# Performance work log

Measured on AMD Instinct MI355X. Metric: run time of the kernel, lower is better.

Reference implementation:

```python
import jax, jax.numpy as jnp
import numpy as np

B, S, H, NH = 2, 2048, 2048, 16
HD = H // NH  # head_dim = 128


def setup_inputs() -> dict:
    key = jax.random.key(0)
    ks = jax.random.split(key, 6)
    scale = 1.0 / np.sqrt(H)
    hidden_state = jax.random.normal(ks[0], (B, S, H), dtype=jnp.float32)
    # upper-triangular (strictly above diagonal) = 1 -> masked positions
    causal_mask = jnp.triu(jnp.ones((S, S), dtype=jnp.float32), k=1)[None, None]
    Wq = jax.random.normal(ks[1], (H, H), dtype=jnp.float32) * scale
    Wk = jax.random.normal(ks[2], (H, H), dtype=jnp.float32) * scale
    Wv = jax.random.normal(ks[3], (H, H), dtype=jnp.float32) * scale
    Wo = jax.random.normal(ks[4], (H, H), dtype=jnp.float32) * scale
    zeros = jnp.zeros((H,), dtype=jnp.float32)
    return {"hidden_state": hidden_state, "causal_mask": causal_mask,
            "Wq": Wq, "bq": zeros, "Wk": Wk, "bk": zeros,
            "Wv": Wv, "bv": zeros, "Wo": Wo, "bo": zeros}


def reference(hidden_state, causal_mask, Wq, bq, Wk, bk, Wv, bv, Wo, bo):
    b, s, h = hidden_state.shape
    q = (hidden_state @ Wq.T + bq).reshape(b, s, NH, HD).transpose(0, 2, 1, 3)  # [B,NH,S,HD]
    k = (hidden_state @ Wk.T + bk).reshape(b, s, NH, HD).transpose(0, 2, 1, 3)
    v = (hidden_state @ Wv.T + bv).reshape(b, s, NH, HD).transpose(0, 2, 1, 3)
    scores = jnp.einsum('bhqd,bhkd->bhqk', q, k) / jnp.sqrt(jnp.float32(HD))
    scores = scores + causal_mask * (-1e9)
    probs = jax.nn.softmax(scores, axis=-1)
    out = jnp.einsum('bhqk,bhkd->bhqd', probs, v)
    out = out.transpose(0, 2, 1, 3).reshape(b, s, h)
    return out @ Wo.T + bo
```

## Files before the change

kernel.cpp:

```cpp
#include <hip/hip_runtime.h>
#include <hip/hip_bf16.h>
#include <stdint.h>

#define B_   2
#define S_   2048
#define H_   2048
#define NH_  16
#define HD_  128
#define MTOT (B_*S_)

typedef __attribute__((ext_vector_type(8))) short bf16x8;
typedef __attribute__((ext_vector_type(4))) float f32x4;

__device__ __forceinline__ void gload_lds16(const void* g, void* l) {
    __builtin_amdgcn_global_load_lds(
        (const __attribute__((address_space(1))) void*)g,
        (__attribute__((address_space(3))) void*)l, 16, 0, 0);
}

__device__ __forceinline__ unsigned short f2bfu(float x) {
    __hip_bfloat16 h = __float2bfloat16(x);
    return *reinterpret_cast<unsigned short*>(&h);
}

__global__ void castk(const float* __restrict__ in, __hip_bfloat16* __restrict__ out, int n4) {
    int i = blockIdx.x * 256 + threadIdx.x;
    if (i < n4) {
        float4 v = *(const float4*)(in + (size_t)i * 4);
        out[(size_t)i*4 + 0] = __float2bfloat16(v.x);
        out[(size_t)i*4 + 1] = __float2bfloat16(v.y);
        out[(size_t)i*4 + 2] = __float2bfloat16(v.z);
        out[(size_t)i*4 + 3] = __float2bfloat16(v.w);
    }
}

__global__ void castw4(const float* __restrict__ w0, const float* __restrict__ w1,
                       const float* __restrict__ w2, const float* __restrict__ w3,
                       __hip_bfloat16* o0, __hip_bfloat16* o1,
                       __hip_bfloat16* o2, __hip_bfloat16* o3, int n4) {
    const float* in; __hip_bfloat16* out;
    switch (blockIdx.y) {
        case 0:  in = w0; out = o0; break;
        case 1:  in = w1; out = o1; break;
        case 2:  in = w2; out = o2; break;
        default: in = w3; out = o3; break;
    }
    int i = blockIdx.x * 256 + threadIdx.x;
    if (i < n4) {
        float4 v = *(const float4*)(in + (size_t)i * 4);
        out[(size_t)i*4 + 0] = __float2bfloat16(v.x);
        out[(size_t)i*4 + 1] = __float2bfloat16(v.y);
        out[(size_t)i*4 + 2] = __float2bfloat16(v.z);
        out[(size_t)i*4 + 3] = __float2bfloat16(v.w);
    }
}

template<int OUT_BF16>
__device__ __forceinline__ void gemm_body(const __hip_bfloat16* __restrict__ Ablk,
                                          const __hip_bfloat16* __restrict__ Wblk,
                                          const float* __restrict__ bias,
                                          void* __restrict__ Cout,
                                          int N, int K, int br, int bc)
{
    __shared__ __align__(16) __hip_bfloat16 As[128 * 32];
    __shared__ __align__(16) __hip_bfloat16 Bs[128 * 32];

    const int tid  = threadIdx.x;
    const int wave = tid >> 6, lane = tid & 63;
    const int quad = lane >> 4, l16 = lane & 15;
    const int wr = wave >> 1, wc = wave & 1;

    f32x4 acc[4][4] = {};

    for (int k0 = 0; k0 < K; k0 += 32) {
#pragma unroll
        for (int t = 0; t < 2; ++t) {
            int c = t * 256 + wave * 64 + lane;
            int row = c >> 2, cc = c & 3;
            int base = (t * 256 + wave * 64) * 16;
            gload_lds16(Ablk + (size_t)row * K + k0 + cc * 8, (char*)As + base);
            gload_lds16(Wblk + (size_t)row * K + k0 + cc * 8, (char*)Bs + base);
        }
        __syncthreads();

        bf16x8 af[4], bf[4];
#pragma unroll
        for (int i = 0; i < 4; ++i)
            af[i] = *(const bf16x8*)&As[(wr * 64 + i * 16 + l16) * 32 + quad * 8];
#pragma unroll
        for (int j = 0; j < 4; ++j)
            bf[j] = *(const bf16x8*)&Bs[(wc * 64 + j * 16 + l16) * 32 + quad * 8];

#pragma unroll
        for (int i = 0; i < 4; ++i)
#pragma unroll
            for (int j = 0; j < 4; ++j)
                acc[i][j] = __builtin_amdgcn_mfma_f32_16x16x32_bf16(af[i], bf[j], acc[i][j], 0, 0, 0);
        __syncthreads();
    }

#pragma unroll
    for (int i = 0; i < 4; ++i) {
        int row = br * 128 + wr * 64 + i * 16 + quad * 4;
#pragma unroll
        for (int j = 0; j < 4; ++j) {
            int col = bc * 128 + wc * 64 + j * 16 + l16;
            float bv = bias[col];
#pragma unroll
            for (int r = 0; r < 4; ++r) {
                float v = acc[i][j][r] + bv;
                if (OUT_BF16)
                    ((__hip_bfloat16*)Cout)[(size_t)(row + r) * N + col] = __float2bfloat16(v);
                else
                    ((float*)Cout)[(size_t)(row + r) * N + col] = v;
            }
        }
    }
}

__global__ __launch_bounds__(256)
void gemm_qkv(const __hip_bfloat16* __restrict__ X,
              const __hip_bfloat16* __restrict__ Wq, const __hip_bfloat16* __restrict__ Wk,
              const __hip_bfloat16* __restrict__ Wv,
              const float* __restrict__ bq, const float* __restrict__ bk,
              const float* __restrict__ bv,
              __hip_bfloat16* Qo, __hip_bfloat16* Ko, __hip_bfloat16* Vo)
{
    const int sel = blockIdx.x >> 4;
    const int bc  = blockIdx.x & 15;
    const int br  = blockIdx.y;
    const __hip_bfloat16* W = (sel == 0) ? Wq : (sel == 1) ? Wk : Wv;
    const float* bias       = (sel == 0) ? bq : (sel == 1) ? bk : bv;
    __hip_bfloat16* out     = (sel == 0) ? Qo : (sel == 1) ? Ko : Vo;
    gemm_body<1>(X + (size_t)(br * 128) * H_, W + (size_t)(bc * 128) * H_,
                 bias, out, H_, H_, br, bc);
}

__global__ __launch_bounds__(256)
void gemm_out(const __hip_bfloat16* __restrict__ A, const __hip_bfloat16* __restrict__ W,
              const float* __restrict__ bias, float* __restrict__ C)
{
    gemm_body<0>(A + (size_t)(blockIdx.y * 128) * H_, W + (size_t)(blockIdx.x * 128) * H_,
                 bias, C, H_, H_, blockIdx.y, blockIdx.x);
}

#define VSTR 72
#define PSTR 72

__global__ __launch_bounds__(256)
void attn_kernel(const __hip_bfloat16* __restrict__ Q,
                 const __hip_bfloat16* __restrict__ K,
                 const __hip_bfloat16* __restrict__ V,
                 __hip_bfloat16* __restrict__ O)
{
    __shared__ __align__(16) char KsB[2][64 * 256];
    __shared__ __align__(16) __hip_bfloat16 VsT[128 * VSTR];
    __shared__ __align__(16) __hip_bfloat16 Ps[4][16 * PSTR];

    const int tid  = threadIdx.x;
    const int wave = tid >> 6, lane = tid & 63;
    const int quad = lane >> 4, l16 = lane & 15;

    const int lid  = blockIdx.x;
    const int xcd  = lid & 7;
    const int slot = lid >> 3;
    const int bh   = ((slot >> 4) << 3) | xcd;
    const int pr   = slot & 15;
    const int b    = bh >> 4, h = bh & 15;

    const size_t headoff = (size_t)b * S_ * H_ + (size_t)h * HD_;
    const __hip_bfloat16* Qp = Q + headoff;
    const __hip_bfloat16* Kp = K + headoff;
    const __hip_bfloat16* Vp = V + headoff;

    const float scale = 0.08838834764831843f;

    for (int which = 0; which < 2; ++which) {
        const int qb = which ? pr : 31 - pr;
        const int qrow_local = wave * 16;
        const int qrow = qb * 64 + qrow_local;

        bf16x8 qf[4];
#pragma unroll
        for (int kd = 0; kd < 4; ++kd)
            qf[kd] = *(const bf16x8*)(Qp + (size_t)(qrow + l16) * H_ + kd * 32 + quad * 8);

        f32x4 oacc[8] = {};
        float mi = -1e30f, li = 0.0f;

        int bb = 0;

        {
#pragma unroll
            for (int t = 0; t < 4; ++t) {
                int c = wave * 256 + t * 64 + lane;
                int row = c >> 4, pos = c & 15;
                int g = pos ^ (row & 7);
                gload_lds16(Kp + (size_t)row * H_ + g * 8, &KsB[0][wave * 4096 + t * 1024]);
            }
            float4 vr[4];
#pragma unroll
            for (int t = 0; t < 4; ++t) {
                int c = t * 256 + tid;
                vr[t] = *(const float4*)(Vp + (size_t)(c & 63) * H_ + (c >> 6) * 8);
            }
            __syncthreads();
#pragma unroll
            for (int t = 0; t < 4; ++t) {
                int c = t * 256 + tid;
                const __hip_bfloat16* vv = (const __hip_bfloat16*)&vr[t];
                int n = c & 63, cc = c >> 6;
#pragma unroll
                for (int i = 0; i < 8; ++i)
                    VsT[(cc * 8 + i) * VSTR + n] = vv[i];
            }
            __syncthreads();
        }

        for (int kb = 0; kb <= qb; ++kb) {
            const bool more = (kb < qb);
            const int nb = bb ^ 1;

            float4 vr2[4];
            if (more) {
                const __hip_bfloat16* Kn = Kp + (size_t)(kb + 1) * 64 * H_;
                const __hip_bfloat16* Vn = Vp + (size_t)(kb + 1) * 64 * H_;
#pragma unroll
                for (int t = 0; t < 4; ++t) {
                    int c = wave * 256 + t * 64 + lane;
                    int row = c >> 4, pos = c & 15;
                    int g = pos ^ (row & 7);
                    gload_lds16(Kn + (size_t)row * H_ + g * 8, &KsB[nb][wave * 4096 + t * 1024]);
                }
#pragma unroll
                for (int t = 0; t < 4; ++t) {
                    int c = t * 256 + tid;
                    vr2[t] = *(const float4*)(Vn + (size_t)(c & 63) * H_ + (c >> 6) * 8);
                }
            }

            f32x4 sacc[4] = {};
#pragma unroll
            for (int cb = 0; cb < 4; ++cb) {
#pragma unroll
                for (int kd = 0; kd < 4; ++kd) {
                    int row = cb * 16 + l16;
                    int pos = (4 * kd + quad) ^ (l16 & 7);
                    bf16x8 kf = *(const bf16x8*)&KsB[bb][row * 256 + pos * 16];
                    sacc[cb] = __builtin_amdgcn_mfma_f32_16x16x32_bf16(kf, qf[kd], sacc[cb], 0, 0, 0);
                }
            }

            const bool diag = (kb == qb);
            float p[4][4];
            float tm = -1e30f;
#pragma unroll
            for (int cb = 0; cb < 4; ++cb)
#pragma unroll
                for (int r = 0; r < 4; ++r) {
                    float s = sacc[cb][r] * scale;
                    if (diag) {
                        int keyl = cb * 16 + quad * 4 + r;
                        if (keyl > qrow_local + l16) s = -1e30f;
                    }
                    p[cb][r] = s;
                    tm = fmaxf(tm, s);
                }
            tm = fmaxf(tm, __shfl_xor(tm, 16));
            tm = fmaxf(tm, __shfl_xor(tm, 32));
            float mnew = fmaxf(mi, tm);
            float sum = 0.0f;
#pragma unroll
            for (int cb = 0; cb < 4; ++cb)
#pragma unroll
                for (int r = 0; r < 4; ++r) {
                    float e = __expf(p[cb][r] - mnew);
                    p[cb][r] = e;
                    sum += e;
                }
            sum += __shfl_xor(sum, 16);
            sum += __shfl_xor(sum, 32);
            float alpha = __expf(mi - mnew);
            li = li * alpha + sum;
            mi = mnew;

            float ar[4];
#pragma unroll
            for (int r = 0; r < 4; ++r)
                ar[r] = __shfl(alpha, quad * 4 + r);
#pragma unroll
            for (int db = 0; db < 8; ++db)
#pragma unroll
                for (int r = 0; r < 4; ++r)
                    oacc[db][r] *= ar[r];

#pragma unroll
            for (int cb = 0; cb < 4; ++cb) {
                ushort4 pk;
                pk.x = f2bfu(p[cb][0]); pk.y = f2bfu(p[cb][1]);
                pk.z = f2bfu(p[cb][2]); pk.w = f2bfu(p[cb][3]);
                *(ushort4*)&Ps[wave][l16 * PSTR + cb * 16 + quad * 4] = pk;
            }

#pragma unroll
            for (int ks = 0; ks < 2; ++ks) {
                bf16x8 pf = *(const bf16x8*)&Ps[wave][l16 * PSTR + ks * 32 + quad * 8];
#pragma unroll
                for (int db = 0; db < 8; ++db) {
                    bf16x8 vf = *(const bf16x8*)&VsT[(db * 16 + l16) * VSTR + ks * 32 + quad * 8];
                    oacc[db] = __builtin_amdgcn_mfma_f32_16x16x32_bf16(pf, vf, oacc[db], 0, 0, 0);
                }
            }

            if (more) {
                __syncthreads();
#pragma unroll
                for (int t = 0; t < 4; ++t) {
                    int c = t * 256 + tid;
                    const __hip_bfloat16* vv = (const __hip_bfloat16*)&vr2[t];
                    int n = c & 63, cc = c >> 6;
#pragma unroll
                    for (int i = 0; i < 8; ++i)
                        VsT[(cc * 8 + i) * VSTR + n] = vv[i];
                }
                __syncthreads();
            }
            bb = nb;
        }

        float lr[4];
#pragma unroll
        for (int r = 0; r < 4; ++r)
            lr[r] = __shfl(li, quad * 4 + r);
#pragma unroll
        for (int db = 0; db < 8; ++db)
#pragma unroll
            for (int r = 0; r < 4; ++r) {
                float v = oacc[db][r] / lr[r];
                size_t row = (size_t)b * S_ + qrow + quad * 4 + r;
                O[row * H_ + h * HD_ + db * 16 + l16] = __float2bfloat16(v);
            }
        __syncthreads();
    }
}

extern "C" void kernel_launch(void* const* d_in, const int* in_sizes, int n_in,
                              void* d_out, int out_size, void* d_ws, size_t ws_size,
                              hipStream_t stream)
{
    const float* hs = (const float*)d_in[0];
    const float* Wq = (const float*)d_in[2];
    const float* bq = (const float*)d_in[3];
    const float* Wk = (const float*)d_in[4];
    const float* bk = (const float*)d_in[5];
    const float* Wv = (const float*)d_in[6];
    const float* bv = (const float*)d_in[7];
    const float* Wo = (const float*)d_in[8];
    const float* bo = (const float*)d_in[9];

    const size_t szX = (size_t)MTOT * H_;
    const size_t szW = (size_t)H_ * H_;

    __hip_bfloat16* Xbf = (__hip_bfloat16*)d_ws;
    __hip_bfloat16* Wqb = Xbf + szX;
    __hip_bfloat16* Wkb = Wqb + szW;
    __hip_bfloat16* Wvb = Wkb + szW;
    __hip_bfloat16* Wob = Wvb + szW;
    __hip_bfloat16* Qb  = Wob + szW;
    __hip_bfloat16* Kb  = Qb + szX;
    __hip_bfloat16* Vb  = Kb + szX;

    castk<<<(int)((szX/4 + 255)/256), 256, 0, stream>>>(hs, Xbf, (int)(szX/4));
    dim3 wgrid((unsigned)((szW/4 + 255)/256), 4);
    castw4<<<wgrid, 256, 0, stream>>>(Wq, Wk, Wv, Wo, Wqb, Wkb, Wvb, Wob, (int)(szW/4));

    gemm_qkv<<<dim3(48, 32), 256, 0, stream>>>(Xbf, Wqb, Wkb, Wvb, bq, bk, bv, Qb, Kb, Vb);

    attn_kernel<<<dim3(512), 256, 0, stream>>>(Qb, Kb, Vb, Xbf);

    gemm_out<<<dim3(16, 32), 256, 0, stream>>>(Xbf, Wob, bo, (float*)d_out);
}
```

Baseline: 418.5 us.

## Write V transposed from QKV GEMM and pass P via cross-lane permute

```diff
diff --git a/kernel.cpp b/kernel.cpp
--- a/kernel.cpp
+++ b/kernel.cpp
@@ -21,6 +21,9 @@
 __device__ __forceinline__ unsigned short f2bfu(float x) {
     __hip_bfloat16 h = __float2bfloat16(x);
     return *reinterpret_cast<unsigned short*>(&h);
+}
+__device__ __forceinline__ int packbf(float a, float b) {
+    return (int)f2bfu(a) | ((int)f2bfu(b) << 16);
 }
 
 __global__ void castk(const float* __restrict__ in, __hip_bfloat16* __restrict__ out, int n4) {
@@ -55,15 +58,16 @@
     }
 }
 
-template<int OUT_BF16>
+template<int SMEMB, int BF16OUT>
 __device__ __forceinline__ void gemm_body(const __hip_bfloat16* __restrict__ Ablk,
                                           const __hip_bfloat16* __restrict__ Wblk,
                                           const float* __restrict__ bias,
                                           void* __restrict__ Cout,
-                                          int N, int K, int br, int bc)
-{
-    __shared__ __align__(16) __hip_bfloat16 As[128 * 32];
-    __shared__ __align__(16) __hip_bfloat16 Bs[128 * 32];
+                                          int N, int K, int br, int bc, bool vt)
+{
+    __shared__ __align__(16) char smem[SMEMB];
+    __hip_bfloat16* As = (__hip_bfloat16*)smem;
+    __hip_bfloat16* Bs = (__hip_bfloat16*)(smem + 8192);
 
     const int tid  = threadIdx.x;
     const int wave = tid >> 6, lane = tid & 63;
@@ -99,6 +103,35 @@
         __syncthreads();
     }
 
+    if (BF16OUT && vt) {
+        __hip_bfloat16* Ls = (__hip_bfloat16*)smem;
+#pragma unroll
+        for (int j = 0; j < 4; ++j) {
+            int d = wc * 64 + j * 16 + l16;
+            float bv = bias[bc * 128 + d];
+#pragma unroll
+            for (int i = 0; i < 4; ++i) {
+                int t0 = wr * 64 + i * 16 + quad * 4;
+#pragma unroll
+                for (int r = 0; r < 4; ++r)
+                    Ls[d * 136 + t0 + r] = __float2bfloat16(acc[i][j][r] + bv);
+            }
+        }
+        __syncthreads();
+        const int bq = br >> 4;
+        const int s0 = (br & 15) * 128;
+        __hip_bfloat16* VT = (__hip_bfloat16*)Cout;
+        const size_t rowbase = (size_t)(bq * 16 + bc) * 128;
+#pragma unroll
+        for (int rep = 0; rep < 8; ++rep) {
+            int L = rep * 256 + tid;
+            int d = L >> 4, tch = L & 15;
+            bf16x8 v = *(const bf16x8*)&Ls[d * 136 + tch * 8];
+            *(bf16x8*)(VT + (rowbase + d) * (size_t)S_ + s0 + tch * 8) = v;
+        }
+        return;
+    }
+
 #pragma unroll
     for (int i = 0; i < 4; ++i) {
         int row = br * 128 + wr * 64 + i * 16 + quad * 4;
@@ -109,7 +142,7 @@
 #pragma unroll
             for (int r = 0; r < 4; ++r) {
                 float v = acc[i][j][r] + bv;
-                if (OUT_BF16)
+                if (BF16OUT)
                     ((__hip_bfloat16*)Cout)[(size_t)(row + r) * N + col] = __float2bfloat16(v);
                 else
                     ((float*)Cout)[(size_t)(row + r) * N + col] = v;
@@ -124,38 +157,34 @@
               const __hip_bfloat16* __restrict__ Wv,
               const float* __restrict__ bq, const float* __restrict__ bk,
               const float* __restrict__ bv,
-              __hip_bfloat16* Qo, __hip_bfloat16* Ko, __hip_bfloat16* Vo)
+              __hip_bfloat16* Qo, __hip_bfloat16* Ko, __hip_bfloat16* VTo)
 {
     const int sel = blockIdx.x >> 4;
     const int bc  = blockIdx.x & 15;
     const int br  = blockIdx.y;
     const __hip_bfloat16* W = (sel == 0) ? Wq : (sel == 1) ? Wk : Wv;
     const float* bias       = (sel == 0) ? bq : (sel == 1) ? bk : bv;
-    __hip_bfloat16* out     = (sel == 0) ? Qo : (sel == 1) ? Ko : Vo;
-    gemm_body<1>(X + (size_t)(br * 128) * H_, W + (size_t)(bc * 128) * H_,
-                 bias, out, H_, H_, br, bc);
+    void* out               = (sel == 0) ? (void*)Qo : (sel == 1) ? (void*)Ko : (void*)VTo;
+    gemm_body<34816, 1>(X + (size_t)(br * 128) * H_, W + (size_t)(bc * 128) * H_,
+                        bias, out, H_, H_, br, bc, sel == 2);
 }
 
 __global__ __launch_bounds__(256)
 void gemm_out(const __hip_bfloat16* __restrict__ A, const __hip_bfloat16* __restrict__ W,
               const float* __restrict__ bias, float* __restrict__ C)
 {
-    gemm_body<0>(A + (size_t)(blockIdx.y * 128) * H_, W + (size_t)(blockIdx.x * 128) * H_,
-                 bias, C, H_, H_, blockIdx.y, blockIdx.x);
-}
-
-#define VSTR 72
-#define PSTR 72
+    gemm_body<16384, 0>(A + (size_t)(blockIdx.y * 128) * H_, W + (size_t)(blockIdx.x * 128) * H_,
+                        bias, C, H_, H_, blockIdx.y, blockIdx.x, false);
+}
 
 __global__ __launch_bounds__(256)
 void attn_kernel(const __hip_bfloat16* __restrict__ Q,
                  const __hip_bfloat16* __restrict__ K,
-                 const __hip_bfloat16* __restrict__ V,
+                 const __hip_bfloat16* __restrict__ VT,
                  __hip_bfloat16* __restrict__ O)
 {
-    __shared__ __align__(16) char KsB[2][64 * 256];
-    __shared__ __align__(16) __hip_bfloat16 VsT[128 * VSTR];
-    __shared__ __align__(16) __hip_bfloat16 Ps[4][16 * PSTR];
+    __shared__ __align__(16) char KsB[2][16384];
+    __shared__ __align__(16) char VtB[2][16384];
 
     const int tid  = threadIdx.x;
     const int wave = tid >> 6, lane = tid & 63;
@@ -171,9 +200,12 @@
     const size_t headoff = (size_t)b * S_ * H_ + (size_t)h * HD_;
     const __hip_bfloat16* Qp = Q + headoff;
     const __hip_bfloat16* Kp = K + headoff;
-    const __hip_bfloat16* Vp = V + headoff;
+    const __hip_bfloat16* Vtp = VT + (size_t)(b * 16 + h) * 128 * S_;
 
     const float scale = 0.08838834764831843f;
+    const int A0 = (((quad & 1) * 2) * 16 + l16) * 4;
+    const int A1 = A0 + 64;
+    const bool hiq = (quad >= 2);
 
     for (int which = 0; which < 2; ++which) {
         const int qb = which ? pr : 31 - pr;
@@ -187,55 +219,34 @@
 
         f32x4 oacc[8] = {};
         float mi = -1e30f, li = 0.0f;
-
         int bb = 0;
 
-        {
-#pragma unroll
-            for (int t = 0; t < 4; ++t) {
-                int c = wave * 256 + t * 64 + lane;
-                int row = c >> 4, pos = c & 15;
-                int g = pos ^ (row & 7);
-                gload_lds16(Kp + (size_t)row * H_ + g * 8, &KsB[0][wave * 4096 + t * 1024]);
-            }
-            float4 vr[4];
-#pragma unroll
-            for (int t = 0; t < 4; ++t) {
-                int c = t * 256 + tid;
-                vr[t] = *(const float4*)(Vp + (size_t)(c & 63) * H_ + (c >> 6) * 8);
-            }
-            __syncthreads();
-#pragma unroll
-            for (int t = 0; t < 4; ++t) {
-                int c = t * 256 + tid;
-                const __hip_bfloat16* vv = (const __hip_bfloat16*)&vr[t];
-                int n = c & 63, cc = c >> 6;
-#pragma unroll
-                for (int i = 0; i < 8; ++i)
-                    VsT[(cc * 8 + i) * VSTR + n] = vv[i];
-            }
-            __syncthreads();
-        }
+#pragma unroll
+        for (int t = 0; t < 4; ++t) {
+            int c = wave * 256 + t * 64 + lane;
+            int krow = c >> 4, kpos = c & 15;
+            gload_lds16(Kp + (size_t)krow * H_ + (kpos ^ (krow & 7)) * 8,
+                        &KsB[0][(wave * 256 + t * 64) * 16]);
+            int vrow = c >> 3, vpos = c & 7;
+            gload_lds16(Vtp + (size_t)vrow * S_ + (vpos ^ (vrow & 7)) * 8,
+                        &VtB[0][(wave * 256 + t * 64) * 16]);
+        }
+        __syncthreads();
 
         for (int kb = 0; kb <= qb; ++kb) {
-            const bool more = (kb < qb);
             const int nb = bb ^ 1;
-
-            float4 vr2[4];
-            if (more) {
+            if (kb < qb) {
                 const __hip_bfloat16* Kn = Kp + (size_t)(kb + 1) * 64 * H_;
-                const __hip_bfloat16* Vn = Vp + (size_t)(kb + 1) * 64 * H_;
+                const int vcol = (kb + 1) * 64;
 #pragma unroll
                 for (int t = 0; t < 4; ++t) {
                     int c = wave * 256 + t * 64 + lane;
-                    int row = c >> 4, pos = c & 15;
-                    int g = pos ^ (row & 7);
-                    gload_lds16(Kn + (size_t)row * H_ + g * 8, &KsB[nb][wave * 4096 + t * 1024]);
-                }
-#pragma unroll
-                for (int t = 0; t < 4; ++t) {
-                    int c = t * 256 + tid;
-                    vr2[t] = *(const float4*)(Vn + (size_t)(c & 63) * H_ + (c >> 6) * 8);
+                    int krow = c >> 4, kpos = c & 15;
+                    gload_lds16(Kn + (size_t)krow * H_ + (kpos ^ (krow & 7)) * 8,
+                                &KsB[nb][(wave * 256 + t * 64) * 16]);
+                    int vrow = c >> 3, vpos = c & 7;
+                    gload_lds16(Vtp + (size_t)vrow * S_ + vcol + (vpos ^ (vrow & 7)) * 8,
+                                &VtB[nb][(wave * 256 + t * 64) * 16]);
                 }
             }
 
@@ -294,37 +305,44 @@
                 for (int r = 0; r < 4; ++r)
                     oacc[db][r] *= ar[r];
 
+            int Pp[4][2];
 #pragma unroll
             for (int cb = 0; cb < 4; ++cb) {
-                ushort4 pk;
-                pk.x = f2bfu(p[cb][0]); pk.y = f2bfu(p[cb][1]);
-                pk.z = f2bfu(p[cb][2]); pk.w = f2bfu(p[cb][3]);
-                *(ushort4*)&Ps[wave][l16 * PSTR + cb * 16 + quad * 4] = pk;
-            }
-
+                Pp[cb][0] = packbf(p[cb][0], p[cb][1]);
+                Pp[cb][1] = packbf(p[cb][2], p[cb][3]);
+            }
+            bf16x8 pf[2];
 #pragma unroll
             for (int ks = 0; ks < 2; ++ks) {
-                bf16x8 pf = *(const bf16x8*)&Ps[wave][l16 * PSTR + ks * 32 + quad * 8];
+                int c0 = 2 * ks, c1 = 2 * ks + 1;
+                int d0 = __builtin_amdgcn_ds_bpermute(A0, Pp[c0][0]);
+                int e0 = __builtin_amdgcn_ds_bpermute(A0, Pp[c1][0]);
+                int d1 = __builtin_amdgcn_ds_bpermute(A0, Pp[c0][1]);
+                int e1 = __builtin_amdgcn_ds_bpermute(A0, Pp[c1][1]);
+                int d2 = __builtin_amdgcn_ds_bpermute(A1, Pp[c0][0]);
+                int e2 = __builtin_amdgcn_ds_bpermute(A1, Pp[c1][0]);
+                int d3 = __builtin_amdgcn_ds_bpermute(A1, Pp[c0][1]);
+                int e3 = __builtin_amdgcn_ds_bpermute(A1, Pp[c1][1]);
+                union { int i[4]; bf16x8 v; } u;
+                u.i[0] = hiq ? e0 : d0;
+                u.i[1] = hiq ? e1 : d1;
+                u.i[2] = hiq ? e2 : d2;
+                u.i[3] = hiq ? e3 : d3;
+                pf[ks] = u.v;
+            }
+
+#pragma unroll
+            for (int ks = 0; ks < 2; ++ks) {
 #pragma unroll
                 for (int db = 0; db < 8; ++db) {
-                    bf16x8 vf = *(const bf16x8*)&VsT[(db * 16 + l16) * VSTR + ks * 32 + quad * 8];
-                    oacc[db] = __builtin_amdgcn_mfma_f32_16x16x32_bf16(pf, vf, oacc[db], 0, 0, 0);
-                }
-            }
-
-            if (more) {
-                __syncthreads();
-#pragma unroll
-                for (int t = 0; t < 4; ++t) {
-                    int c = t * 256 + tid;
-                    const __hip_bfloat16* vv = (const __hip_bfloat16*)&vr2[t];
-                    int n = c & 63, cc = c >> 6;
-#pragma unroll
-                    for (int i = 0; i < 8; ++i)
-                        VsT[(cc * 8 + i) * VSTR + n] = vv[i];
-                }
-                __syncthreads();
-            }
+                    int vrow = db * 16 + l16;
+                    int vpos = (ks * 4 + quad) ^ (l16 & 7);
+                    bf16x8 vf = *(const bf16x8*)&VtB[bb][vrow * 128 + vpos * 16];
+                    oacc[db] = __builtin_amdgcn_mfma_f32_16x16x32_bf16(pf[ks], vf, oacc[db], 0, 0, 0);
+                }
+            }
+
+            __syncthreads();
             bb = nb;
         }
 
@@ -340,7 +358,6 @@
                 size_t row = (size_t)b * S_ + qrow + quad * 4 + r;
                 O[row * H_ + h * HD_ + db * 16 + l16] = __float2bfloat16(v);
             }
-        __syncthreads();
     }
 }
 
@@ -368,15 +385,15 @@
     __hip_bfloat16* Wob = Wvb + szW;
     __hip_bfloat16* Qb  = Wob + szW;
     __hip_bfloat16* Kb  = Qb + szX;
-    __hip_bfloat16* Vb  = Kb + szX;
+    __hip_bfloat16* VTb = Kb + szX;
 
     castk<<<(int)((szX/4 + 255)/256), 256, 0, stream>>>(hs, Xbf, (int)(szX/4));
     dim3 wgrid((unsigned)((szW/4 + 255)/256), 4);
     castw4<<<wgrid, 256, 0, stream>>>(Wq, Wk, Wv, Wo, Wqb, Wkb, Wvb, Wob, (int)(szW/4));
 
-    gemm_qkv<<<dim3(48, 32), 256, 0, stream>>>(Xbf, Wqb, Wkb, Wvb, bq, bk, bv, Qb, Kb, Vb);
-
-    attn_kernel<<<dim3(512), 256, 0, stream>>>(Qb, Kb, Vb, Xbf);
+    gemm_qkv<<<dim3(48, 32), 256, 0, stream>>>(Xbf, Wqb, Wkb, Wvb, bq, bk, bv, Qb, Kb, VTb);
+
+    attn_kernel<<<dim3(512), 256, 0, stream>>>(Qb, Kb, VTb, Xbf);
 
     gemm_out<<<dim3(16, 32), 256, 0, stream>>>(Xbf, Wob, bo, (float*)d_out);
 }
```

Measured after the change: 422.1 us. No clear change (+0.9%).
